# Performance work log

Measured on AMD Instinct MI355X. Metric: run time of the kernel, lower is better.

Reference implementation:

```python
import jax, jax.numpy as jnp
import numpy as np

N, K, DIM = 50000, 16, 256
SLOPE = 0.2

def _leaky(x):
    return jnp.where(x >= 0, x, SLOPE * x)

def _mlp(x, w, b):
    # torch nn.Linear followed by LeakyReLU(0.2); w is [in, out]
    return _leaky(x @ w + b)

def setup_inputs() -> dict:
    key = jax.random.key(0)
    ks = jax.random.split(key, 14)
    d4, d2 = DIM // 4, DIM // 2
    def lin(k, i, o):
        kw, kb = jax.random.split(k)
        s = 1.0 / np.sqrt(i)
        return (jax.random.uniform(kw, (i, o), jnp.float32, -s, s),
                jax.random.uniform(kb, (o,), jnp.float32, -s, s))
    w_res, b_res = lin(ks[0], DIM, DIM)
    w_init, b_init = lin(ks[1], DIM, d4)
    w_g1, b_g1 = lin(ks[2], 4, d4)
    w_g2, b_g2 = lin(ks[3], 4, d2)
    w_fin, b_fin = lin(ks[4], DIM, DIM)
    return {
        "input_features": jax.random.normal(ks[5], (N, DIM), jnp.float32),
        "geom_features": jax.random.normal(ks[6], (N, K, 4), jnp.float32),
        "closest_indices": jax.random.randint(ks[7], (N, K), 0, N, jnp.int32),
        "w_res": w_res, "b_res": b_res,
        "w_init": w_init, "b_init": b_init,
        "w_g1": w_g1, "b_g1": b_g1,
        "w_g2": w_g2, "b_g2": b_g2,
        "w_fin": w_fin, "b_fin": b_fin,
    }

def _lfa(feat, geom, idx, w_g, b_g):
    # feat: [N, d]; geom: [N, K, 4]; idx: [N, K]
    g = _mlp(geom, w_g, b_g)                 # [N, K, d]
    gathered = feat[idx]                      # [N, K, d] gather over points
    combined = jnp.concatenate([g, gathered], axis=-1)  # [N, K, 2d]
    return jnp.mean(combined, axis=1)         # [N, 2d]

def reference(input_features, geom_features, closest_indices,
              w_res, b_res, w_init, b_init, w_g1, b_g1, w_g2, b_g2,
              w_fin, b_fin):
    residual = _mlp(input_features, w_res, b_res)            # [N, DIM]
    a = _mlp(input_features, w_init, b_init)                 # [N, DIM/4]
    a = _lfa(a, geom_features, closest_indices, w_g1, b_g1)  # [N, DIM/2]
    a = _lfa(a, geom_features, closest_indices, w_g2, b_g2)  # [N, DIM]
    a = _mlp(a, w_fin, b_fin)                                # [N, DIM]
    return a + residual
```

## Files before the change

### kernel.cpp

```cpp
#include <hip/hip_runtime.h>

#define DIM 256
#define KNN 16
#define SLOPE 0.2f

typedef unsigned short u16;
typedef __attribute__((ext_vector_type(8))) unsigned short u16x8;
typedef __attribute__((ext_vector_type(4))) unsigned short u16x4;
typedef __attribute__((ext_vector_type(8))) short s16x8;
typedef __attribute__((ext_vector_type(4))) float f32x4;

__device__ __forceinline__ float leaky(float x) { return x >= 0.f ? x : SLOPE * x; }
__device__ __forceinline__ u16 f2bu(float f) {
    unsigned int u = __float_as_uint(f);
    u = (u + 0x7FFFu + ((u >> 16) & 1u)) >> 16;
    return (u16)u;
}
__device__ __forceinline__ float bu2f(u16 h) {
    return __uint_as_float(((unsigned int)h) << 16);
}

__global__ __launch_bounds__(256) void k_prep(
    const float* __restrict__ w_res, const float* __restrict__ w_init,
    const float* __restrict__ w_fin, u16* __restrict__ wT1, u16* __restrict__ wT3)
{
    const int c = blockIdx.x, t = threadIdx.x;
    if (c < 256)      wT1[c * 256 + t] = f2bu(w_res[t * 256 + c]);
    else if (c < 320) wT1[c * 256 + t] = f2bu(w_init[t * 64 + (c - 256)]);
    else              wT3[(c - 320) * 256 + t] = f2bu(w_fin[t * 256 + (c - 320)]);
}

#define APAD 264
#define BPAD 40
__global__ __launch_bounds__(256) void k_gemm1(
    const float* __restrict__ in, const u16* __restrict__ wT1,
    const float* __restrict__ b_res, const float* __restrict__ b_init,
    float* __restrict__ resid, u16* __restrict__ a1, int N)
{
    __shared__ u16 A_s[64 * APAD];
    __shared__ u16 B_s[320 * BPAD];
    const int t = threadIdx.x;
    const int base = blockIdx.x * 64;

    {
        const int row = t >> 2, seg = t & 3;
        const int grow = min(base + row, N - 1);
        const float* src = in + (size_t)grow * DIM + seg * 64;
        u16* dst = &A_s[row * APAD + seg * 64];
        #pragma unroll
        for (int j = 0; j < 8; ++j) {
            float4 f0 = *(const float4*)(src + j * 8);
            float4 f1 = *(const float4*)(src + j * 8 + 4);
            u16x8 p;
            p[0] = f2bu(f0.x); p[1] = f2bu(f0.y); p[2] = f2bu(f0.z); p[3] = f2bu(f0.w);
            p[4] = f2bu(f1.x); p[5] = f2bu(f1.y); p[6] = f2bu(f1.z); p[7] = f2bu(f1.w);
            *(u16x8*)(dst + j * 8) = p;
        }
    }

    f32x4 acc[4][5];
    #pragma unroll
    for (int i = 0; i < 4; ++i)
        #pragma unroll
        for (int j = 0; j < 5; ++j)
            acc[i][j] = (f32x4){0.f, 0.f, 0.f, 0.f};

    const int w = t >> 6, lane = t & 63;
    const int llow = lane & 15, lhi = lane >> 4;

    for (int ks = 0; ks < 8; ++ks) {
        u16x8 breg[5];
        #pragma unroll
        for (int j = 0; j < 5; ++j) {
            int id = t + 256 * j;
            int col = id >> 2, kg = id & 3;
            breg[j] = *(const u16x8*)(wT1 + col * 256 + ks * 32 + kg * 8);
        }
        __syncthreads();
        #pragma unroll
        for (int j = 0; j < 5; ++j) {
            int id = t + 256 * j;
            int col = id >> 2, kg = id & 3;
            *(u16x8*)(&B_s[col * BPAD + kg * 8]) = breg[j];
        }
        __syncthreads();

        s16x8 afrag[4];
        #pragma unroll
        for (int rt = 0; rt < 4; ++rt)
            afrag[rt] = *(const s16x8*)(&A_s[(rt * 16 + llow) * APAD + ks * 32 + lhi * 8]);
        #pragma unroll
        for (int ci = 0; ci < 5; ++ci) {
            const int ct = w * 5 + ci;
            s16x8 bfrag = *(const s16x8*)(&B_s[(ct * 16 + llow) * BPAD + lhi * 8]);
            #pragma unroll
            for (int rt = 0; rt < 4; ++rt)
                acc[rt][ci] = __builtin_amdgcn_mfma_f32_16x16x32_bf16(
                    afrag[rt], bfrag, acc[rt][ci], 0, 0, 0);
        }
    }

    #pragma unroll
    for (int ci = 0; ci < 5; ++ci) {
        const int ct = w * 5 + ci;
        const int col = ct * 16 + llow;
        if (col < 256) {
            const float bias = b_res[col];
            #pragma unroll
            for (int rt = 0; rt < 4; ++rt)
                #pragma unroll
                for (int r = 0; r < 4; ++r) {
                    int row = base + rt * 16 + lhi * 4 + r;
                    if (row < N)
                        resid[(size_t)row * DIM + col] = leaky(acc[rt][ci][r] + bias);
                }
        } else {
            const int c2 = col - 256;
            const float bias = b_init[c2];
            #pragma unroll
            for (int rt = 0; rt < 4; ++rt)
                #pragma unroll
                for (int r = 0; r < 4; ++r) {
                    int row = base + rt * 16 + lhi * 4 + r;
                    if (row < N)
                        a1[(size_t)row * 64 + c2] = f2bu(leaky(acc[rt][ci][r] + bias));
                }
        }
    }
}

__global__ __launch_bounds__(256) void k_lfa1(
    const float* __restrict__ geom, const int* __restrict__ idx,
    const float* __restrict__ w_g1, const float* __restrict__ b_g1,
    const u16* __restrict__ a1, u16* __restrict__ a2, int N)
{
    __shared__ float geom_s[16 * KNN * 4];
    __shared__ int idx_s[16 * KNN];
    const int t = threadIdx.x;
    const int base = blockIdx.x * 16;

    {
        size_t off = (size_t)base * 64 + t * 4;
        size_t mx = (size_t)N * 64 - 4;
        if (off > mx) off = mx;
        *(float4*)&geom_s[t * 4] = *(const float4*)(geom + off);
        int io = base * KNN + t;
        if (t < 256) idx_s[t] = idx[min(io, N * KNN - 1)];
    }
    __syncthreads();

    const int pt = t >> 4, s = t & 15;
    const int n = base + pt;

    float wr[4][4], bb[4];
    #pragma unroll
    for (int r = 0; r < 4; ++r)
        #pragma unroll
        for (int j = 0; j < 4; ++j)
            wr[r][j] = w_g1[r * 64 + s * 4 + j];
    #pragma unroll
    for (int j = 0; j < 4; ++j) bb[j] = b_g1[s * 4 + j];

    float accM[4] = {0.f, 0.f, 0.f, 0.f};
    const float4* g4 = (const float4*)&geom_s[pt * 64];
    #pragma unroll
    for (int k = 0; k < KNN; ++k) {
        float4 g = g4[k];
        #pragma unroll
        for (int j = 0; j < 4; ++j)
            accM[j] += leaky(g.x * wr[0][j] + g.y * wr[1][j] + g.z * wr[2][j] + g.w * wr[3][j] + bb[j]);
    }

    float accG[4] = {0.f, 0.f, 0.f, 0.f};
    #pragma unroll
    for (int k = 0; k < KNN; ++k) {
        u16x4 u = *(const u16x4*)(a1 + (size_t)idx_s[pt * KNN + k] * 64 + s * 4);
        #pragma unroll
        for (int j = 0; j < 4; ++j) accG[j] += bu2f(u[j]);
    }

    if (n < N) {
        u16x4 pm, pg;
        #pragma unroll
        for (int j = 0; j < 4; ++j) {
            pm[j] = f2bu(accM[j] * 0.0625f);
            pg[j] = f2bu(accG[j] * 0.0625f);
        }
        *(u16x4*)(a2 + (size_t)n * 128 + s * 4) = pm;
        *(u16x4*)(a2 + (size_t)n * 128 + 64 + s * 4) = pg;
    }
}

__global__ __launch_bounds__(256) void k_lfa2_fin(
    const float* __restrict__ geom, const int* __restrict__ idx,
    const float* __restrict__ w_g2, const float* __restrict__ b_g2,
    const u16* __restrict__ a2, const u16* __restrict__ wT3,
    const float* __restrict__ b_fin, float* __restrict__ out, int N)
{
    __shared__ u16 a3_s[64 * APAD];
    __shared__ u16 B_s[256 * BPAD];
    __shared__ float geom_s[64 * KNN * 4];
    __shared__ int idx_s[64 * KNN];
    const int t = threadIdx.x;
    const int base = blockIdx.x * 64;

    {
        size_t mx = (size_t)N * 64 - 4;
        #pragma unroll
        for (int j = 0; j < 4; ++j) {
            size_t off = (size_t)base * 64 + t * 4 + j * 1024;
            if (off > mx) off = mx;
            *(float4*)&geom_s[t * 4 + j * 1024] = *(const float4*)(geom + off);
        }
        int imx = N * KNN - 1;
        #pragma unroll
        for (int j = 0; j < 4; ++j) {
            int off = base * KNN + t + j * 256;
            idx_s[t + j * 256] = idx[min(off, imx)];
        }
    }
    __syncthreads();

    {
        const int c = t & 127, h = t >> 7;
        const float w0 = w_g2[c], w1 = w_g2[128 + c], w2 = w_g2[256 + c],
                    w3 = w_g2[384 + c], bb = b_g2[c];
        for (int p = 0; p < 32; ++p) {
            const int pt = h * 32 + p;
            float acc = 0.f;
            const float4* g4 = (const float4*)&geom_s[pt * 64];
            #pragma unroll
            for (int k = 0; k < KNN; ++k) {
                float4 g = g4[k];
                acc += leaky(g.x * w0 + g.y * w1 + g.z * w2 + g.w * w3 + bb);
            }
            a3_s[pt * APAD + c] = f2bu(acc * 0.0625f);
        }
    }
    {
        const int pt = t >> 2, q = t & 3;
        float acc[32];
        #pragma unroll
        for (int j = 0; j < 32; ++j) acc[j] = 0.f;
        for (int k = 0; k < KNN; ++k) {
            const u16* row = a2 + (size_t)idx_s[pt * KNN + k] * 128 + q * 32;
            #pragma unroll
            for (int v = 0; v < 4; ++v) {
                u16x8 u = *(const u16x8*)(row + v * 8);
                #pragma unroll
                for (int j = 0; j < 8; ++j) acc[v * 8 + j] += bu2f(u[j]);
            }
        }
        #pragma unroll
        for (int v = 0; v < 4; ++v) {
            u16x8 p;
            #pragma unroll
            for (int j = 0; j < 8; ++j) p[j] = f2bu(acc[v * 8 + j] * 0.0625f);
            *(u16x8*)(&a3_s[pt * APAD + 128 + q * 32 + v * 8]) = p;
        }
    }

    f32x4 acc[4][4];
    #pragma unroll
    for (int i = 0; i < 4; ++i)
        #pragma unroll
        for (int j = 0; j < 4; ++j)
            acc[i][j] = (f32x4){0.f, 0.f, 0.f, 0.f};

    const int w = t >> 6, lane = t & 63;
    const int llow = lane & 15, lhi = lane >> 4;

    for (int ks = 0; ks < 8; ++ks) {
        u16x8 breg[4];
        #pragma unroll
        for (int kg = 0; kg < 4; ++kg)
            breg[kg] = *(const u16x8*)(wT3 + t * 256 + ks * 32 + kg * 8);
        __syncthreads();
        #pragma unroll
        for (int kg = 0; kg < 4; ++kg)
            *(u16x8*)(&B_s[t * BPAD + kg * 8]) = breg[kg];
        __syncthreads();

        s16x8 afrag[4];
        #pragma unroll
        for (int rt = 0; rt < 4; ++rt)
            afrag[rt] = *(const s16x8*)(&a3_s[(rt * 16 + llow) * APAD + ks * 32 + lhi * 8]);
        #pragma unroll
        for (int ci = 0; ci < 4; ++ci) {
            const int ct = w * 4 + ci;
            s16x8 bfrag = *(const s16x8*)(&B_s[(ct * 16 + llow) * BPAD + lhi * 8]);
            #pragma unroll
            for (int rt = 0; rt < 4; ++rt)
                acc[rt][ci] = __builtin_amdgcn_mfma_f32_16x16x32_bf16(
                    afrag[rt], bfrag, acc[rt][ci], 0, 0, 0);
        }
    }

    #pragma unroll
    for (int ci = 0; ci < 4; ++ci) {
        const int ct = w * 4 + ci;
        const int col = ct * 16 + llow;
        const float bias = b_fin[col];
        #pragma unroll
        for (int rt = 0; rt < 4; ++rt)
            #pragma unroll
            for (int r = 0; r < 4; ++r) {
                int row = base + rt * 16 + lhi * 4 + r;
                if (row < N) {
                    size_t o = (size_t)row * DIM + col;
                    out[o] = leaky(acc[rt][ci][r] + bias) + out[o];
                }
            }
    }
}

extern "C" void kernel_launch(void* const* d_in, const int* in_sizes, int n_in,
                              void* d_out, int out_size, void* d_ws, size_t ws_size,
                              hipStream_t stream) {
    const float* in    = (const float*)d_in[0];
    const float* geom  = (const float*)d_in[1];
    const int*   idx   = (const int*)d_in[2];
    const float* w_res = (const float*)d_in[3];
    const float* b_res = (const float*)d_in[4];
    const float* w_init= (const float*)d_in[5];
    const float* b_init= (const float*)d_in[6];
    const float* w_g1  = (const float*)d_in[7];
    const float* b_g1  = (const float*)d_in[8];
    const float* w_g2  = (const float*)d_in[9];
    const float* b_g2  = (const float*)d_in[10];
    const float* w_fin = (const float*)d_in[11];
    const float* b_fin = (const float*)d_in[12];
    float* out = (float*)d_out;

    const int N = in_sizes[0] / DIM;

    char* ws = (char*)d_ws;
    u16* a1  = (u16*)ws;
    u16* a2  = (u16*)(ws + (size_t)N * 64 * 2);
    u16* wT1 = (u16*)(ws + (size_t)N * (64 + 128) * 2);
    u16* wT3 = wT1 + 320 * 256;

    k_prep<<<576, 256, 0, stream>>>(w_res, w_init, w_fin, wT1, wT3);
    k_gemm1<<<(N + 63) / 64, 256, 0, stream>>>(in, wT1, b_res, b_init, out, a1, N);
    k_lfa1<<<(N + 15) / 16, 256, 0, stream>>>(geom, idx, w_g1, b_g1, a1, a2, N);
    k_lfa2_fin<<<(N + 63) / 64, 256, 0, stream>>>(geom, idx, w_g2, b_g2, a2, wT3, b_fin, out, N);
}
```

Baseline: 295.2 us.

## Pre-swizzle weights into MFMA fragment layout and load B fragments directly from global

The weight-prep kernel now writes bf16 weights in the exact per-lane MFMA B-fragment order, so the GEMM kernels read each B fragment with one 16-byte global load per lane. This removes the per-k-step shared-memory staging of B, the two barriers per iteration, and the B_s shared buffers, which lowers LDS use and may raise occupancy. The cost is that each wave fetches its B fragments from global/L2 with no block-level sharing, and load latency is exposed without explicit prefetching.

```diff
diff --git a/kernel.cpp b/kernel.cpp
--- a/kernel.cpp
+++ b/kernel.cpp
@@ -24,21 +24,41 @@
     const float* __restrict__ w_res, const float* __restrict__ w_init,
     const float* __restrict__ w_fin, u16* __restrict__ wT1, u16* __restrict__ wT3)
 {
-    const int c = blockIdx.x, t = threadIdx.x;
-    if (c < 256)      wT1[c * 256 + t] = f2bu(w_res[t * 256 + c]);
-    else if (c < 320) wT1[c * 256 + t] = f2bu(w_init[t * 64 + (c - 256)]);
-    else              wT3[(c - 320) * 256 + t] = f2bu(w_fin[t * 256 + (c - 320)]);
+    const int t = blockIdx.x * 256 + threadIdx.x;
+    if (t < 20 * 8 * 64) {
+        const int lane = t & 63, frag = t >> 6;
+        const int ks = frag & 7, ct = frag >> 3;
+        const int col = ct * 16 + (lane & 15);
+        const int k0 = ks * 32 + (lane >> 4) * 8;
+        u16x8 p;
+        #pragma unroll
+        for (int j = 0; j < 8; ++j) {
+            float v = (col < 256) ? w_res[(size_t)(k0 + j) * 256 + col]
+                                  : w_init[(size_t)(k0 + j) * 64 + (col - 256)];
+            p[j] = f2bu(v);
+        }
+        *(u16x8*)(wT1 + (size_t)t * 8) = p;
+    } else if (t < 20 * 8 * 64 + 16 * 8 * 64) {
+        const int u = t - 20 * 8 * 64;
+        const int lane = u & 63, frag = u >> 6;
+        const int ks = frag & 7, ct = frag >> 3;
+        const int col = ct * 16 + (lane & 15);
+        const int k0 = ks * 32 + (lane >> 4) * 8;
+        u16x8 p;
+        #pragma unroll
+        for (int j = 0; j < 8; ++j)
+            p[j] = f2bu(w_fin[(size_t)(k0 + j) * 256 + col]);
+        *(u16x8*)(wT3 + (size_t)u * 8) = p;
+    }
 }
 
 #define APAD 264
-#define BPAD 40
 __global__ __launch_bounds__(256) void k_gemm1(
     const float* __restrict__ in, const u16* __restrict__ wT1,
     const float* __restrict__ b_res, const float* __restrict__ b_init,
     float* __restrict__ resid, u16* __restrict__ a1, int N)
 {
     __shared__ u16 A_s[64 * APAD];
-    __shared__ u16 B_s[320 * BPAD];
     const int t = threadIdx.x;
     const int base = blockIdx.x * 64;
 
@@ -57,6 +77,7 @@
             *(u16x8*)(dst + j * 8) = p;
         }
     }
+    __syncthreads();
 
     f32x4 acc[4][5];
     #pragma unroll
@@ -69,35 +90,22 @@
     const int llow = lane & 15, lhi = lane >> 4;
 
     for (int ks = 0; ks < 8; ++ks) {
-        u16x8 breg[5];
-        #pragma unroll
-        for (int j = 0; j < 5; ++j) {
-            int id = t + 256 * j;
-            int col = id >> 2, kg = id & 3;
-            breg[j] = *(const u16x8*)(wT1 + col * 256 + ks * 32 + kg * 8);
-        }
-        __syncthreads();
-        #pragma unroll
-        for (int j = 0; j < 5; ++j) {
-            int id = t + 256 * j;
-            int col = id >> 2, kg = id & 3;
-            *(u16x8*)(&B_s[col * BPAD + kg * 8]) = breg[j];
-        }
-        __syncthreads();
-
+        s16x8 bfrag[5];
+        #pragma unroll
+        for (int ci = 0; ci < 5; ++ci) {
+            const int ct = w * 5 + ci;
+            bfrag[ci] = *(const s16x8*)(wT1 + ((size_t)(ct * 8 + ks) * 64 + lane) * 8);
+        }
         s16x8 afrag[4];
         #pragma unroll
         for (int rt = 0; rt < 4; ++rt)
             afrag[rt] = *(const s16x8*)(&A_s[(rt * 16 + llow) * APAD + ks * 32 + lhi * 8]);
         #pragma unroll
-        for (int ci = 0; ci < 5; ++ci) {
-            const int ct = w * 5 + ci;
-            s16x8 bfrag = *(const s16x8*)(&B_s[(ct * 16 + llow) * BPAD + lhi * 8]);
+        for (int ci = 0; ci < 5; ++ci)
             #pragma unroll
             for (int rt = 0; rt < 4; ++rt)
                 acc[rt][ci] = __builtin_amdgcn_mfma_f32_16x16x32_bf16(
-                    afrag[rt], bfrag, acc[rt][ci], 0, 0, 0);
-        }
+                    afrag[rt], bfrag[ci], acc[rt][ci], 0, 0, 0);
     }
 
     #pragma unroll
@@ -198,7 +206,6 @@
     const float* __restrict__ b_fin, float* __restrict__ out, int N)
 {
     __shared__ u16 a3_s[64 * APAD];
-    __shared__ u16 B_s[256 * BPAD];
     __shared__ float geom_s[64 * KNN * 4];
     __shared__ int idx_s[64 * KNN];
     const int t = threadIdx.x;
@@ -259,6 +266,7 @@
             *(u16x8*)(&a3_s[pt * APAD + 128 + q * 32 + v * 8]) = p;
         }
     }
+    __syncthreads();
 
     f32x4 acc[4][4];
     #pragma unroll
@@ -271,29 +279,22 @@
     const int llow = lane & 15, lhi = lane >> 4;
 
     for (int ks = 0; ks < 8; ++ks) {
-        u16x8 breg[4];
-        #pragma unroll
-        for (int kg = 0; kg < 4; ++kg)
-            breg[kg] = *(const u16x8*)(wT3 + t * 256 + ks * 32 + kg * 8);
-        __syncthreads();
-        #pragma unroll
-        for (int kg = 0; kg < 4; ++kg)
-            *(u16x8*)(&B_s[t * BPAD + kg * 8]) = breg[kg];
-        __syncthreads();
-
+        s16x8 bfrag[4];
+        #pragma unroll
+        for (int ci = 0; ci < 4; ++ci) {
+            const int ct = w * 4 + ci;
+            bfrag[ci] = *(const s16x8*)(wT3 + ((size_t)(ct * 8 + ks) * 64 + lane) * 8);
+        }
         s16x8 afrag[4];
         #pragma unroll
         for (int rt = 0; rt < 4; ++rt)
             afrag[rt] = *(const s16x8*)(&a3_s[(rt * 16 + llow) * APAD + ks * 32 + lhi * 8]);
         #pragma unroll
-        for (int ci = 0; ci < 4; ++ci) {
-            const int ct = w * 4 + ci;
-            s16x8 bfrag = *(const s16x8*)(&B_s[(ct * 16 + llow) * BPAD + lhi * 8]);
+        for (int ci = 0; ci < 4; ++ci)
             #pragma unroll
             for (int rt = 0; rt < 4; ++rt)
                 acc[rt][ci] = __builtin_amdgcn_mfma_f32_16x16x32_bf16(
-                    afrag[rt], bfrag, acc[rt][ci], 0, 0, 0);
-        }
+                    afrag[rt], bfrag[ci], acc[rt][ci], 0, 0, 0);
     }
 
     #pragma unroll
@@ -340,7 +341,7 @@
     u16* wT1 = (u16*)(ws + (size_t)N * (64 + 128) * 2);
     u16* wT3 = wT1 + 320 * 256;
 
-    k_prep<<<576, 256, 0, stream>>>(w_res, w_init, w_fin, wT1, wT3);
+    k_prep<<<72, 256, 0, stream>>>(w_res, w_init, w_fin, wT1, wT3);
     k_gemm1<<<(N + 63) / 64, 256, 0, stream>>>(in, wT1, b_res, b_init, out, a1, N);
     k_lfa1<<<(N + 15) / 16, 256, 0, stream>>>(geom, idx, w_g1, b_g1, a1, a2, N);
     k_lfa2_fin<<<(N + 63) / 64, 256, 0, stream>>>(geom, idx, w_g2, b_g2, a2, wT3, b_fin, out, N);
```

New measurement: 296.9 us. About the same (+0.6%).
